# Performance work log

Measured on AMD Instinct MI355X. Metric: run time of the kernel, lower is better.

## Reference

```python
import jax, jax.numpy as jnp
import numpy as np

MASK_DENSITY = 0.1  # fraction of nonzero weights kept by the sparsity mask


def setup_inputs() -> dict:
    key = jax.random.key(0)
    k_data, k_w, k_m, k_b = jax.random.split(key, 4)
    tokens, in_f, out_f = 8192, 4096, 4096
    data = jax.random.normal(k_data, (tokens, in_f), dtype=jnp.float32)
    weight = jax.random.normal(k_w, (out_f, in_f), dtype=jnp.float32)
    mask = (jax.random.uniform(k_m, (out_f, in_f)) < MASK_DENSITY).astype(jnp.float32)
    bias = jax.random.normal(k_b, (out_f,), dtype=jnp.float32)
    return {"data": data, "weight": weight, "mask": mask, "bias": bias}


def reference(data, weight, mask, bias):
    # out = data @ (mask * weight)^T + bias  (sparse linear; CSR of mask*weight
    # in the original kernel -- dense math is identical).
    w_sp = mask * weight                      # [out_f, in_f]
    out = jnp.einsum("ti,oi->to", data, w_sp) # [tokens, out_f]
    return out + bias
```

## Files before the change

kernel.cpp:

```cpp
#include <hip/hip_runtime.h>
#include <hip/hip_bf16.h>


#define GM 8192
#define GN 4096
#define GK 4096
#define NT (GK / 64)

typedef __attribute__((ext_vector_type(8))) short short8;
typedef __attribute__((ext_vector_type(8))) short bf16x8;
typedef __attribute__((ext_vector_type(4))) float f32x4;

__device__ __forceinline__ short f2bf(float x) {
    unsigned u = __builtin_bit_cast(unsigned, x);
    u += 0x7fffu + ((u >> 16) & 1u);
    return (short)(u >> 16);
}

__device__ __forceinline__ void stage16(const short* g, short* l) {
    __builtin_amdgcn_global_load_lds(
        (const __attribute__((address_space(1))) unsigned int*)g,
        (__attribute__((address_space(3))) unsigned int*)l, 16, 0, 0);
}

__global__ void cvt_data_kernel(const float* __restrict__ in, short* __restrict__ out, long n) {
    long i0 = ((long)blockIdx.x * blockDim.x + threadIdx.x) * 8;
    long stride = (long)gridDim.x * blockDim.x * 8;
    for (long i = i0; i < n; i += stride) {
        float4 a = *(const float4*)(in + i);
        float4 b = *(const float4*)(in + i + 4);
        short8 o;
        o[0] = f2bf(a.x); o[1] = f2bf(a.y); o[2] = f2bf(a.z); o[3] = f2bf(a.w);
        o[4] = f2bf(b.x); o[5] = f2bf(b.y); o[6] = f2bf(b.z); o[7] = f2bf(b.w);
        *(short8*)(out + i) = o;
    }
}

__global__ void cvt_w_kernel(const float* __restrict__ w, const float* __restrict__ m,
                             short* __restrict__ out, long n) {
    long i0 = ((long)blockIdx.x * blockDim.x + threadIdx.x) * 8;
    long stride = (long)gridDim.x * blockDim.x * 8;
    for (long i = i0; i < n; i += stride) {
        float4 wa = *(const float4*)(w + i);
        float4 wb = *(const float4*)(w + i + 4);
        float4 ma = *(const float4*)(m + i);
        float4 mb = *(const float4*)(m + i + 4);
        short8 o;
        o[0] = f2bf(wa.x * ma.x); o[1] = f2bf(wa.y * ma.y);
        o[2] = f2bf(wa.z * ma.z); o[3] = f2bf(wa.w * ma.w);
        o[4] = f2bf(wb.x * mb.x); o[5] = f2bf(wb.y * mb.y);
        o[6] = f2bf(wb.z * mb.z); o[7] = f2bf(wb.w * mb.w);
        *(short8*)(out + i) = o;
    }
}

__global__ __launch_bounds__(512, 2) void gemm_8w(const short* __restrict__ A,
                                                  const short* __restrict__ B,
                                                  const float* __restrict__ bias,
                                                  float* __restrict__ C) {
    __shared__ short lds[65536];

    const int tid  = threadIdx.x;
    const int lane = tid & 63;
    const int wid  = tid >> 6;
    const int wr   = wid >> 2;
    const int wc   = wid & 3;

    const int bid  = blockIdx.x;
    const int swz  = (bid & 7) * 64 + (bid >> 3);
    const int brow = (swz >> 4) << 8;
    const int bcol = (swz & 15) << 8;

    const int trow = tid >> 2;
    const int qlog = (tid & 3) ^ ((((trow >> 3) & 1) << 1) | ((trow >> 1) & 1));

    const int l15 = lane & 15;
    const int q   = lane >> 4;
    const int qx  = (((l15 >> 3) & 1) << 1) | ((l15 >> 1) & 1);
    const int foff = l15 * 32 + ((q ^ qx) << 3);
    const int aW = wr * 4096;
    const int bW = wc * 2048;

    f32x4 acc[8][4] = {};
    bf16x8 af[4], bfr[4];

    auto stA = [&](int kb, int sb, size_t kcol) {
        #pragma unroll
        for (int j = 0; j < 2; ++j)
            stage16(A + (size_t)(brow + j * 128 + trow) * GK + kcol + kb * 32 + qlog * 8,
                    &lds[sb + kb * 8192 + j * 4096 + wid * 512]);
    };
    auto stB = [&](int kb, int sb, size_t kcol) {
        #pragma unroll
        for (int j = 0; j < 2; ++j)
            stage16(B + (size_t)(bcol + j * 128 + trow) * GK + kcol + kb * 32 + qlog * 8,
                    &lds[sb + 16384 + kb * 8192 + j * 4096 + wid * 512]);
    };

    stA(0, 0, 0); stB(0, 0, 0); stA(1, 0, 0); stB(1, 0, 0);
    asm volatile("s_waitcnt vmcnt(4)" ::: "memory");
    __builtin_amdgcn_s_barrier();
    asm volatile("" ::: "memory");

#define PHASE(KB, MH, VMSTMT, STGSTMT)                                            \
  {                                                                                \
    VMSTMT;                                                                        \
    _Pragma("unroll")                                                              \
    for (int m = 0; m < 4; ++m)                                                    \
      af[m] = *(const bf16x8*)&lds[cb + (KB) * 8192 + aW + ((MH) * 4 + m) * 512 + foff]; \
    if ((MH) == 0) {                                                               \
      _Pragma("unroll")                                                            \
      for (int n = 0; n < 4; ++n)                                                  \
        bfr[n] = *(const bf16x8*)&lds[cb + 16384 + (KB) * 8192 + bW + n * 512 + foff]; \
    }                                                                              \
    STGSTMT;                                                                       \
    __builtin_amdgcn_s_barrier();                                                  \
    asm volatile("s_waitcnt lgkmcnt(0)" ::: "memory");                             \
    __builtin_amdgcn_sched_barrier(0);                                             \
    __builtin_amdgcn_s_setprio(1);                                                 \
    _Pragma("unroll")                                                              \
    for (int m = 0; m < 4; ++m)                                                    \
      _Pragma("unroll")                                                            \
      for (int n = 0; n < 4; ++n)                                                  \
        acc[(MH) * 4 + m][n] = __builtin_amdgcn_mfma_f32_16x16x32_bf16(            \
            af[m], bfr[n], acc[(MH) * 4 + m][n], 0, 0, 0);                         \
    __builtin_amdgcn_s_setprio(0);                                                 \
    __builtin_amdgcn_s_barrier();                                                  \
    asm volatile("" ::: "memory");                                                 \
  }

    for (int T = 0; T < NT; ++T) {
        const int cb = (T & 1) << 15;
        const int sb = 32768 - cb;
        const size_t kn = (size_t)(T + 1) * 64;
        const bool st = (T + 1 < NT);

        PHASE(0, 0, , if (st) stA(0, sb, kn))
        PHASE(0, 1,
              if (st) { asm volatile("s_waitcnt vmcnt(2)" ::: "memory"); }
              else    { asm volatile("s_waitcnt vmcnt(0)" ::: "memory"); },
              if (st) stB(0, sb, kn))
        PHASE(1, 0, , if (st) stA(1, sb, kn))
        PHASE(1, 1,
              if (st) { asm volatile("s_waitcnt vmcnt(2)" ::: "memory"); }
              else    { asm volatile("s_waitcnt vmcnt(0)" ::: "memory"); },
              if (st) stB(1, sb, kn))
    }
#undef PHASE

    #pragma unroll
    for (int n = 0; n < 4; ++n) {
        const int col = bcol + wc * 64 + n * 16 + l15;
        const float bv = bias[col];
        #pragma unroll
        for (int m = 0; m < 8; ++m) {
            const int rowb = brow + wr * 128 + m * 16 + (q << 2);
            #pragma unroll
            for (int r = 0; r < 4; ++r)
                C[(size_t)(rowb + r) * GN + col] = acc[m][n][r] + bv;
        }
    }
}

extern "C" void kernel_launch(void* const* d_in, const int* in_sizes, int n_in,
                              void* d_out, int out_size, void* d_ws, size_t ws_size,
                              hipStream_t stream) {
    const float* data   = (const float*)d_in[0];
    const float* weight = (const float*)d_in[1];
    const float* mask   = (const float*)d_in[2];
    const float* bias   = (const float*)d_in[3];
    float* out = (float*)d_out;

    short* dataB = (short*)d_ws;
    short* wB    = dataB + (size_t)GM * GK;

    cvt_data_kernel<<<2048, 256, 0, stream>>>(data, dataB, (long)GM * GK);
    cvt_w_kernel<<<2048, 256, 0, stream>>>(weight, mask, wB, (long)GN * GK);

    gemm_8w<<<512, 512, 0, stream>>>(dataB, wB, bias, out);
}
```

Baseline: 298.2 us.

## Double-buffer MFMA fragments in registers to overlap LDS reads with compute

Splits the A and B fragment registers into two sets so that each phase issues the LDS reads for the next phase before running its MFMAs on the current set. The explicit lgkmcnt(0) wait and one workgroup barrier per phase are removed, and the global-load vmcnt waits move to after the MFMA block. The goal is to hide LDS read latency behind matrix math and cut synchronisation stalls. The cost is more live vector registers under a tight launch bound, which could cause spills or lower occupancy.

Measured after the change: 306.9 us. 1.03x slower.

```diff
diff --git a/kernel.cpp b/kernel.cpp
--- a/kernel.cpp
+++ b/kernel.cpp
@@ -82,7 +82,7 @@
     const int bW = wc * 2048;
 
     f32x4 acc[8][4] = {};
-    bf16x8 af[4], bfr[4];
+    bf16x8 af0[4], af1[4], bf0[4], bf1[4];
 
     auto stA = [&](int kb, int sb, size_t kcol) {
         #pragma unroll
@@ -101,32 +101,27 @@
     asm volatile("s_waitcnt vmcnt(4)" ::: "memory");
     __builtin_amdgcn_s_barrier();
     asm volatile("" ::: "memory");
-
-#define PHASE(KB, MH, VMSTMT, STGSTMT)                                            \
-  {                                                                                \
-    VMSTMT;                                                                        \
-    _Pragma("unroll")                                                              \
-    for (int m = 0; m < 4; ++m)                                                    \
-      af[m] = *(const bf16x8*)&lds[cb + (KB) * 8192 + aW + ((MH) * 4 + m) * 512 + foff]; \
-    if ((MH) == 0) {                                                               \
-      _Pragma("unroll")                                                            \
-      for (int n = 0; n < 4; ++n)                                                  \
-        bfr[n] = *(const bf16x8*)&lds[cb + 16384 + (KB) * 8192 + bW + n * 512 + foff]; \
-    }                                                                              \
-    STGSTMT;                                                                       \
-    __builtin_amdgcn_s_barrier();                                                  \
-    asm volatile("s_waitcnt lgkmcnt(0)" ::: "memory");                             \
-    __builtin_amdgcn_sched_barrier(0);                                             \
-    __builtin_amdgcn_s_setprio(1);                                                 \
-    _Pragma("unroll")                                                              \
-    for (int m = 0; m < 4; ++m)                                                    \
-      _Pragma("unroll")                                                            \
-      for (int n = 0; n < 4; ++n)                                                  \
-        acc[(MH) * 4 + m][n] = __builtin_amdgcn_mfma_f32_16x16x32_bf16(            \
-            af[m], bfr[n], acc[(MH) * 4 + m][n], 0, 0, 0);                         \
-    __builtin_amdgcn_s_setprio(0);                                                 \
-    __builtin_amdgcn_s_barrier();                                                  \
-    asm volatile("" ::: "memory");                                                 \
+    #pragma unroll
+    for (int m = 0; m < 4; ++m) af0[m] = *(const bf16x8*)&lds[aW + m * 512 + foff];
+    #pragma unroll
+    for (int n = 0; n < 4; ++n) bf0[n] = *(const bf16x8*)&lds[16384 + bW + n * 512 + foff];
+
+#define PHASE(RDSTMT, STGSTMT, AFSET, BFSET, MH, VMSTMT)                           \
+  {                                                                                 \
+    RDSTMT;                                                                         \
+    STGSTMT;                                                                        \
+    __builtin_amdgcn_sched_barrier(0);                                              \
+    __builtin_amdgcn_s_setprio(1);                                                  \
+    _Pragma("unroll")                                                               \
+    for (int m = 0; m < 4; ++m)                                                     \
+      _Pragma("unroll")                                                             \
+      for (int n = 0; n < 4; ++n)                                                   \
+        acc[(MH) * 4 + m][n] = __builtin_amdgcn_mfma_f32_16x16x32_bf16(             \
+            AFSET[m], BFSET[n], acc[(MH) * 4 + m][n], 0, 0, 0);                     \
+    __builtin_amdgcn_s_setprio(0);                                                  \
+    VMSTMT;                                                                         \
+    __builtin_amdgcn_s_barrier();                                                   \
+    asm volatile("" ::: "memory");                                                  \
   }
 
     for (int T = 0; T < NT; ++T) {
@@ -135,16 +130,45 @@
         const size_t kn = (size_t)(T + 1) * 64;
         const bool st = (T + 1 < NT);
 
-        PHASE(0, 0, , if (st) stA(0, sb, kn))
-        PHASE(0, 1,
-              if (st) { asm volatile("s_waitcnt vmcnt(2)" ::: "memory"); }
-              else    { asm volatile("s_waitcnt vmcnt(0)" ::: "memory"); },
-              if (st) stB(0, sb, kn))
-        PHASE(1, 0, , if (st) stA(1, sb, kn))
-        PHASE(1, 1,
-              if (st) { asm volatile("s_waitcnt vmcnt(2)" ::: "memory"); }
-              else    { asm volatile("s_waitcnt vmcnt(0)" ::: "memory"); },
-              if (st) stB(1, sb, kn))
+        PHASE(
+            { _Pragma("unroll")
+              for (int m = 0; m < 4; ++m)
+                  af1[m] = *(const bf16x8*)&lds[cb + aW + (4 + m) * 512 + foff]; },
+            if (st) stA(0, sb, kn),
+            af0, bf0, 0,
+            if (st) { asm volatile("s_waitcnt vmcnt(2)" ::: "memory"); }
+            else    { asm volatile("s_waitcnt vmcnt(0)" ::: "memory"); })
+
+        PHASE(
+            { _Pragma("unroll")
+              for (int m = 0; m < 4; ++m)
+                  af0[m] = *(const bf16x8*)&lds[cb + 8192 + aW + m * 512 + foff];
+              _Pragma("unroll")
+              for (int n = 0; n < 4; ++n)
+                  bf1[n] = *(const bf16x8*)&lds[cb + 16384 + 8192 + bW + n * 512 + foff]; },
+            if (st) stB(0, sb, kn),
+            af1, bf0, 1, )
+
+        PHASE(
+            { _Pragma("unroll")
+              for (int m = 0; m < 4; ++m)
+                  af1[m] = *(const bf16x8*)&lds[cb + 8192 + aW + (4 + m) * 512 + foff]; },
+            if (st) stA(1, sb, kn),
+            af0, bf1, 0,
+            if (st) { asm volatile("s_waitcnt vmcnt(2)" ::: "memory"); }
+            else    { asm volatile("s_waitcnt vmcnt(0)" ::: "memory"); })
+
+        PHASE(
+            if (st) {
+              _Pragma("unroll")
+              for (int m = 0; m < 4; ++m)
+                  af0[m] = *(const bf16x8*)&lds[sb + aW + m * 512 + foff];
+              _Pragma("unroll")
+              for (int n = 0; n < 4; ++n)
+                  bf0[n] = *(const bf16x8*)&lds[sb + 16384 + bW + n * 512 + foff];
+            },
+            if (st) stB(1, sb, kn),
+            af1, bf1, 1, )
     }
 #undef PHASE
 
```

## Restructure GEMM main loop into 8-phase pipeline with staggered A/B prefetch

Applied to the files above, without the earlier changes.

Rewrites the K-loop to process two 64-wide K tiles per iteration in eight phases. Each phase covers both K sub-blocks for two M fragments, and B fragments are loaded once per tile. A and B staging are decoupled: B is prefetched a tile further ahead into the opposite buffer, and A loads are spread across phases with partial lgkm waits. The goal is better overlap of global-to-LDS copies with MFMA and fewer fragment reloads. The cost is more barriers per tile and a tricky buffer-reuse schedule that risks races.

After: 307.8 us. +3.2%, slower.

```diff
diff --git a/kernel.cpp b/kernel.cpp
--- a/kernel.cpp
+++ b/kernel.cpp
@@ -6,6 +6,7 @@
 #define GN 4096
 #define GK 4096
 #define NT (GK / 64)
+#define NI (NT / 2)
 
 typedef __attribute__((ext_vector_type(8))) short short8;
 typedef __attribute__((ext_vector_type(8))) short bf16x8;
@@ -82,71 +83,83 @@
     const int bW = wc * 2048;
 
     f32x4 acc[8][4] = {};
-    bf16x8 af[4], bfr[4];
+    bf16x8 af[4], bfr[8];
 
-    auto stA = [&](int kb, int sb, size_t kcol) {
+    auto stA = [&](int kb, int dbase, size_t kcol) {
         #pragma unroll
         for (int j = 0; j < 2; ++j)
             stage16(A + (size_t)(brow + j * 128 + trow) * GK + kcol + kb * 32 + qlog * 8,
-                    &lds[sb + kb * 8192 + j * 4096 + wid * 512]);
+                    &lds[dbase + kb * 8192 + j * 4096 + wid * 512]);
     };
-    auto stB = [&](int kb, int sb, size_t kcol) {
+    auto stB = [&](int kb, int dbase, size_t kcol) {
         #pragma unroll
         for (int j = 0; j < 2; ++j)
             stage16(B + (size_t)(bcol + j * 128 + trow) * GK + kcol + kb * 32 + qlog * 8,
-                    &lds[sb + 16384 + kb * 8192 + j * 4096 + wid * 512]);
+                    &lds[dbase + 16384 + kb * 8192 + j * 4096 + wid * 512]);
     };
 
-    stA(0, 0, 0); stB(0, 0, 0); stA(1, 0, 0); stB(1, 0, 0);
+    stA(0, 0, 0); stA(1, 0, 0);
+    stB(0, 0, 0); stB(1, 0, 0);
+    stB(0, 32768, 64); stB(1, 32768, 64);
     asm volatile("s_waitcnt vmcnt(4)" ::: "memory");
     __builtin_amdgcn_s_barrier();
     asm volatile("" ::: "memory");
 
-#define PHASE(KB, MH, VMSTMT, STGSTMT)                                            \
-  {                                                                                \
-    VMSTMT;                                                                        \
-    _Pragma("unroll")                                                              \
-    for (int m = 0; m < 4; ++m)                                                    \
-      af[m] = *(const bf16x8*)&lds[cb + (KB) * 8192 + aW + ((MH) * 4 + m) * 512 + foff]; \
-    if ((MH) == 0) {                                                               \
-      _Pragma("unroll")                                                            \
-      for (int n = 0; n < 4; ++n)                                                  \
-        bfr[n] = *(const bf16x8*)&lds[cb + 16384 + (KB) * 8192 + bW + n * 512 + foff]; \
-    }                                                                              \
-    STGSTMT;                                                                       \
-    __builtin_amdgcn_s_barrier();                                                  \
-    asm volatile("s_waitcnt lgkmcnt(0)" ::: "memory");                             \
-    __builtin_amdgcn_sched_barrier(0);                                             \
-    __builtin_amdgcn_s_setprio(1);                                                 \
-    _Pragma("unroll")                                                              \
-    for (int m = 0; m < 4; ++m)                                                    \
-      _Pragma("unroll")                                                            \
-      for (int n = 0; n < 4; ++n)                                                  \
-        acc[(MH) * 4 + m][n] = __builtin_amdgcn_mfma_f32_16x16x32_bf16(            \
-            af[m], bfr[n], acc[(MH) * 4 + m][n], 0, 0, 0);                         \
-    __builtin_amdgcn_s_setprio(0);                                                 \
-    __builtin_amdgcn_s_barrier();                                                  \
-    asm volatile("" ::: "memory");                                                 \
+#define PH(DB, QD, LOADB, STG, LGKM8, VM)                                          \
+  {                                                                                 \
+    _Pragma("unroll")                                                               \
+    for (int mm = 0; mm < 2; ++mm)                                                  \
+      _Pragma("unroll")                                                             \
+      for (int kb = 0; kb < 2; ++kb)                                                \
+        af[mm * 2 + kb] =                                                           \
+            *(const bf16x8*)&lds[(DB) + kb * 8192 + aW + ((QD) * 2 + mm) * 512 + foff]; \
+    if (LOADB) {                                                                    \
+      _Pragma("unroll")                                                             \
+      for (int n = 0; n < 4; ++n)                                                   \
+        _Pragma("unroll")                                                           \
+        for (int kb = 0; kb < 2; ++kb)                                              \
+          bfr[n * 2 + kb] =                                                         \
+              *(const bf16x8*)&lds[(DB) + 16384 + kb * 8192 + bW + n * 512 + foff]; \
+    }                                                                               \
+    STG;                                                                            \
+    if (LGKM8) { asm volatile("s_waitcnt lgkmcnt(8)" ::: "memory"); }               \
+    __builtin_amdgcn_s_barrier();                                                   \
+    asm volatile("s_waitcnt lgkmcnt(0)" ::: "memory");                              \
+    __builtin_amdgcn_sched_barrier(0);                                              \
+    __builtin_amdgcn_s_setprio(1);                                                  \
+    _Pragma("unroll")                                                               \
+    for (int mm = 0; mm < 2; ++mm)                                                  \
+      _Pragma("unroll")                                                             \
+      for (int n = 0; n < 4; ++n)                                                   \
+        _Pragma("unroll")                                                           \
+        for (int kb = 0; kb < 2; ++kb)                                              \
+          acc[(QD) * 2 + mm][n] = __builtin_amdgcn_mfma_f32_16x16x32_bf16(          \
+              af[mm * 2 + kb], bfr[n * 2 + kb], acc[(QD) * 2 + mm][n], 0, 0, 0);    \
+    __builtin_amdgcn_s_setprio(0);                                                  \
+    VM;                                                                             \
+    __builtin_amdgcn_s_barrier();                                                   \
+    asm volatile("" ::: "memory");                                                  \
   }
 
-    for (int T = 0; T < NT; ++T) {
-        const int cb = (T & 1) << 15;
-        const int sb = 32768 - cb;
-        const size_t kn = (size_t)(T + 1) * 64;
-        const bool st = (T + 1 < NT);
+    for (int i = 0; i < NI; ++i) {
+        const bool st = (i + 1 < NI);
+        const size_t k1 = (size_t)(2 * i + 1) * 64;
+        const size_t k2 = (size_t)(2 * i + 2) * 64;
+        const size_t k3 = (size_t)(2 * i + 3) * 64;
 
-        PHASE(0, 0, , if (st) stA(0, sb, kn))
-        PHASE(0, 1,
-              if (st) { asm volatile("s_waitcnt vmcnt(2)" ::: "memory"); }
-              else    { asm volatile("s_waitcnt vmcnt(0)" ::: "memory"); },
-              if (st) stB(0, sb, kn))
-        PHASE(1, 0, , if (st) stA(1, sb, kn))
-        PHASE(1, 1,
-              if (st) { asm volatile("s_waitcnt vmcnt(2)" ::: "memory"); }
-              else    { asm volatile("s_waitcnt vmcnt(0)" ::: "memory"); },
-              if (st) stB(1, sb, kn))
+        PH(0, 0, true,  { stA(0, 32768, k1); stA(1, 32768, k1); }, true, )
+        PH(0, 1, false, { if (st) stB(0, 0, k2); }, false, )
+        PH(0, 2, false, { if (st) stB(1, 0, k2); }, false, )
+        PH(0, 3, false, { }, false,
+           if (st) { asm volatile("s_waitcnt vmcnt(4)" ::: "memory"); }
+           else    { asm volatile("s_waitcnt vmcnt(0)" ::: "memory"); })
+        PH(32768, 0, true,  { if (st) { stA(0, 0, k2); stA(1, 0, k2); } }, true, )
+        PH(32768, 1, false, { if (st) stB(0, 32768, k3); }, false, )
+        PH(32768, 2, false, { if (st) stB(1, 32768, k3); }, false, )
+        PH(32768, 3, false, { }, false,
+           if (st) { asm volatile("s_waitcnt vmcnt(4)" ::: "memory"); })
     }
-#undef PHASE
+#undef PH
 
     #pragma unroll
     for (int n = 0; n < 4; ++n) {
```

## Pre-swizzle weights into MFMA fragment layout and load B directly from global

Applied to the files above, without the earlier changes.

The weight conversion kernel now writes the masked bf16 weights in a fragment-major layout so each wave can load its B operands with coalesced 16-byte global loads straight into registers. This removes B staging through LDS, halving shared memory use, and the main loop is restructured to double-buffer B in registers while issuing A-fragment LDS reads interleaved with MFMA quarters. It also cuts barriers per K tile. The cost is more VGPR pressure, and B is now read from global (mostly L2) by every wave instead of being shared through LDS, so there is more redundant global traffic across the 4 row-waves.

Result: slower. 363.9 us (+22.0%).

```diff
diff --git a/kernel.cpp b/kernel.cpp
--- a/kernel.cpp
+++ b/kernel.cpp
@@ -37,28 +37,34 @@
 }
 
 __global__ void cvt_w_kernel(const float* __restrict__ w, const float* __restrict__ m,
-                             short* __restrict__ out, long n) {
-    long i0 = ((long)blockIdx.x * blockDim.x + threadIdx.x) * 8;
-    long stride = (long)gridDim.x * blockDim.x * 8;
-    for (long i = i0; i < n; i += stride) {
-        float4 wa = *(const float4*)(w + i);
-        float4 wb = *(const float4*)(w + i + 4);
-        float4 ma = *(const float4*)(m + i);
-        float4 mb = *(const float4*)(m + i + 4);
+                             short* __restrict__ out) {
+    long t0 = (long)blockIdx.x * blockDim.x + threadIdx.x;
+    long stride = (long)gridDim.x * blockDim.x;
+    for (long t = t0; t < 4096L * 512; t += stride) {
+        const int col = (int)(t >> 9);
+        const int ko8 = (int)(t & 511);
+        const float* wp = w + (size_t)col * GK + ko8 * 8;
+        const float* mp = m + (size_t)col * GK + ko8 * 8;
+        float4 wa = *(const float4*)wp;
+        float4 wb = *(const float4*)(wp + 4);
+        float4 ma = *(const float4*)mp;
+        float4 mb = *(const float4*)(mp + 4);
         short8 o;
         o[0] = f2bf(wa.x * ma.x); o[1] = f2bf(wa.y * ma.y);
         o[2] = f2bf(wa.z * ma.z); o[3] = f2bf(wa.w * ma.w);
         o[4] = f2bf(wb.x * mb.x); o[5] = f2bf(wb.y * mb.y);
         o[6] = f2bf(wb.z * mb.z); o[7] = f2bf(wb.w * mb.w);
-        *(short8*)(out + i) = o;
+        size_t oi = ((size_t)((col >> 4) * 128 + (ko8 >> 2)) * 64
+                     + ((ko8 & 3) * 16 + (col & 15))) * 8;
+        *(short8*)(out + oi) = o;
     }
 }
 
 __global__ __launch_bounds__(512, 2) void gemm_8w(const short* __restrict__ A,
-                                                  const short* __restrict__ B,
+                                                  const short* __restrict__ Bt,
                                                   const float* __restrict__ bias,
                                                   float* __restrict__ C) {
-    __shared__ short lds[65536];
+    __shared__ short lds[32768];
 
     const int tid  = threadIdx.x;
     const int lane = tid & 63;
@@ -79,74 +85,83 @@
     const int qx  = (((l15 >> 3) & 1) << 1) | ((l15 >> 1) & 1);
     const int foff = l15 * 32 + ((q ^ qx) << 3);
     const int aW = wr * 4096;
-    const int bW = wc * 2048;
+
+    const int co0 = (bcol >> 4) + wc * 4;
+    const short* btb = Bt + (size_t)co0 * 65536 + lane * 8;
 
     f32x4 acc[8][4] = {};
-    bf16x8 af[4], bfr[4];
+    bf16x8 af0[4], af1[4], bA[8], bB[8];
 
-    auto stA = [&](int kb, int sb, size_t kcol) {
+    auto stA = [&](int kb, int dbase, size_t kcol) {
         #pragma unroll
         for (int j = 0; j < 2; ++j)
             stage16(A + (size_t)(brow + j * 128 + trow) * GK + kcol + kb * 32 + qlog * 8,
-                    &lds[sb + kb * 8192 + j * 4096 + wid * 512]);
-    };
-    auto stB = [&](int kb, int sb, size_t kcol) {
-        #pragma unroll
-        for (int j = 0; j < 2; ++j)
-            stage16(B + (size_t)(bcol + j * 128 + trow) * GK + kcol + kb * 32 + qlog * 8,
-                    &lds[sb + 16384 + kb * 8192 + j * 4096 + wid * 512]);
+                    &lds[dbase + kb * 8192 + j * 4096 + wid * 512]);
     };
 
-    stA(0, 0, 0); stB(0, 0, 0); stA(1, 0, 0); stB(1, 0, 0);
-    asm volatile("s_waitcnt vmcnt(4)" ::: "memory");
+#define RDQ(DST, DB, QD)                                                           \
+    _Pragma("unroll")                                                              \
+    for (int mm = 0; mm < 2; ++mm)                                                 \
+      _Pragma("unroll")                                                            \
+      for (int kb = 0; kb < 2; ++kb)                                               \
+        DST[mm * 2 + kb] =                                                         \
+            *(const bf16x8*)&lds[(DB) + kb * 8192 + aW + ((QD) * 2 + mm) * 512 + foff];
+
+#define BLD(DST, T)                                                                \
+    _Pragma("unroll")                                                              \
+    for (int n = 0; n < 4; ++n)                                                    \
+      _Pragma("unroll")                                                            \
+      for (int kb = 0; kb < 2; ++kb)                                               \
+        DST[n * 2 + kb] =                                                          \
+            *(const bf16x8*)(btb + (size_t)n * 65536 + (size_t)(2 * (T) + kb) * 512);
+
+#define MFMAQ(QD, AF, BC)                                                          \
+    __builtin_amdgcn_s_setprio(1);                                                 \
+    _Pragma("unroll")                                                              \
+    for (int mm = 0; mm < 2; ++mm)                                                 \
+      _Pragma("unroll")                                                            \
+      for (int n = 0; n < 4; ++n)                                                  \
+        _Pragma("unroll")                                                          \
+        for (int kb = 0; kb < 2; ++kb)                                             \
+          acc[(QD) * 2 + mm][n] = __builtin_amdgcn_mfma_f32_16x16x32_bf16(         \
+              AF[mm * 2 + kb], BC[n * 2 + kb], acc[(QD) * 2 + mm][n], 0, 0, 0);    \
+    __builtin_amdgcn_s_setprio(0);
+
+#define TILE(T, DB, DBN, BC, BN)                                                   \
+  {                                                                                 \
+    const bool st = (T) + 1 < NT;                                                   \
+    const size_t kn = (size_t)((T) + 1) * 64;                                       \
+    RDQ(af0, DB, 0)                                                                 \
+    RDQ(af1, DB, 1)                                                                 \
+    if (st) { stA(0, DBN, kn); stA(1, DBN, kn); BLD(BN, (T) + 1) }                  \
+    __builtin_amdgcn_sched_barrier(0);                                              \
+    MFMAQ(0, af0, BC)                                                               \
+    RDQ(af0, DB, 2)                                                                 \
+    __builtin_amdgcn_sched_barrier(0);                                              \
+    MFMAQ(1, af1, BC)                                                               \
+    RDQ(af1, DB, 3)                                                                 \
+    __builtin_amdgcn_sched_barrier(0);                                              \
+    MFMAQ(2, af0, BC)                                                               \
+    MFMAQ(3, af1, BC)                                                               \
+    asm volatile("s_waitcnt vmcnt(0)" ::: "memory");                                \
+    __builtin_amdgcn_s_barrier();                                                   \
+    asm volatile("" ::: "memory");                                                  \
+  }
+
+    stA(0, 0, 0); stA(1, 0, 0);
+    BLD(bA, 0)
+    asm volatile("s_waitcnt vmcnt(0)" ::: "memory");
     __builtin_amdgcn_s_barrier();
     asm volatile("" ::: "memory");
 
-#define PHASE(KB, MH, VMSTMT, STGSTMT)                                            \
-  {                                                                                \
-    VMSTMT;                                                                        \
-    _Pragma("unroll")                                                              \
-    for (int m = 0; m < 4; ++m)                                                    \
-      af[m] = *(const bf16x8*)&lds[cb + (KB) * 8192 + aW + ((MH) * 4 + m) * 512 + foff]; \
-    if ((MH) == 0) {                                                               \
-      _Pragma("unroll")                                                            \
-      for (int n = 0; n < 4; ++n)                                                  \
-        bfr[n] = *(const bf16x8*)&lds[cb + 16384 + (KB) * 8192 + bW + n * 512 + foff]; \
-    }                                                                              \
-    STGSTMT;                                                                       \
-    __builtin_amdgcn_s_barrier();                                                  \
-    asm volatile("s_waitcnt lgkmcnt(0)" ::: "memory");                             \
-    __builtin_amdgcn_sched_barrier(0);                                             \
-    __builtin_amdgcn_s_setprio(1);                                                 \
-    _Pragma("unroll")                                                              \
-    for (int m = 0; m < 4; ++m)                                                    \
-      _Pragma("unroll")                                                            \
-      for (int n = 0; n < 4; ++n)                                                  \
-        acc[(MH) * 4 + m][n] = __builtin_amdgcn_mfma_f32_16x16x32_bf16(            \
-            af[m], bfr[n], acc[(MH) * 4 + m][n], 0, 0, 0);                         \
-    __builtin_amdgcn_s_setprio(0);                                                 \
-    __builtin_amdgcn_s_barrier();                                                  \
-    asm volatile("" ::: "memory");                                                 \
-  }
-
-    for (int T = 0; T < NT; ++T) {
-        const int cb = (T & 1) << 15;
-        const int sb = 32768 - cb;
-        const size_t kn = (size_t)(T + 1) * 64;
-        const bool st = (T + 1 < NT);
-
-        PHASE(0, 0, , if (st) stA(0, sb, kn))
-        PHASE(0, 1,
-              if (st) { asm volatile("s_waitcnt vmcnt(2)" ::: "memory"); }
-              else    { asm volatile("s_waitcnt vmcnt(0)" ::: "memory"); },
-              if (st) stB(0, sb, kn))
-        PHASE(1, 0, , if (st) stA(1, sb, kn))
-        PHASE(1, 1,
-              if (st) { asm volatile("s_waitcnt vmcnt(2)" ::: "memory"); }
-              else    { asm volatile("s_waitcnt vmcnt(0)" ::: "memory"); },
-              if (st) stB(1, sb, kn))
+    for (int T = 0; T < NT; T += 2) {
+        TILE(T,     0,     16384, bA, bB)
+        TILE(T + 1, 16384, 0,     bB, bA)
     }
-#undef PHASE
+#undef TILE
+#undef MFMAQ
+#undef BLD
+#undef RDQ
 
     #pragma unroll
     for (int n = 0; n < 4; ++n) {
@@ -172,10 +187,10 @@
     float* out = (float*)d_out;
 
     short* dataB = (short*)d_ws;
-    short* wB    = dataB + (size_t)GM * GK;
+    short* wBt   = dataB + (size_t)GM * GK;
 
     cvt_data_kernel<<<2048, 256, 0, stream>>>(data, dataB, (long)GM * GK);
-    cvt_w_kernel<<<2048, 256, 0, stream>>>(weight, mask, wB, (long)GN * GK);
+    cvt_w_kernel<<<2048, 256, 0, stream>>>(weight, mask, wBt);
 
-    gemm_8w<<<512, 512, 0, stream>>>(dataB, wB, bias, out);
+    gemm_8w<<<512, 512, 0, stream>>>(dataB, wBt, bias, out);
 }
```
